# Performance work log

Hardware: AMD Instinct MI355X
Metric: run time of the kernel (lower is better)

The kernel has to match this reference:

```python
import jax, jax.numpy as jnp
import numpy as np


def setup_inputs() -> dict:
    key = jax.random.key(0)
    B, C, T, F = 16, 2, 1000, 257
    k1, = jax.random.split(key, 1)
    inp = jax.random.normal(k1, (B, C, T, F, 2), dtype=jnp.float32)
    weights = jnp.ones((1, C, 1, F, 1), dtype=jnp.float32)   # init constant 1
    bias = jnp.zeros((1, C, 1, F, 1), dtype=jnp.float32)     # init constant 0
    alpha = jnp.full((1, C, F, 1), -4.0, dtype=jnp.float32)  # init constant -4
    s_1 = jnp.zeros((B, C, F, 1), dtype=jnp.float32)
    return {"input": inp, "weights": weights, "bias": bias, "alpha": alpha, "s_1": s_1}


def reference(input, weights, bias, alpha, s_1):
    # input: [B, C, T, F, 2]
    in_data2 = jnp.sum(input ** 2, axis=-1, keepdims=True)  # [B, C, T, F, 1]
    a = jax.nn.sigmoid(alpha)                               # [1, C, F, 1]

    def step(s, x):
        s = s * (1.0 - a) + x * a   # EMA over time, per (c, f)
        return s, s

    # scan over time axis -> move T to leading axis
    xs = jnp.moveaxis(in_data2, 2, 0)          # [T, B, C, F, 1]
    s_last, smooth = jax.lax.scan(step, s_1, xs)
    smooth = jnp.sqrt(jnp.moveaxis(smooth, 0, 2))  # [B, C, T, F, 1]

    res = input / (smooth + 1e-8) * weights + bias
    return res, s_last
```

## Files before the change

### kernel.cpp

```cpp
#include <hip/hip_runtime.h>

#define BB 16
#define CC 2
#define TT 1000
#define FF 257
#define NCHAIN (BB * CC * FF)
#define RES_ELEMS ((size_t)BB * CC * TT * FF * 2)

#define CPB 16
#define KCH 20
#define LCH 50

__global__ __launch_bounds__(320, 3) void fnorm_kernel(
    const float* __restrict__ input,
    const float* __restrict__ weights,
    const float* __restrict__ bias,
    const float* __restrict__ alpha,
    const float* __restrict__ s1,
    float* __restrict__ out)
{
    const int tx = threadIdx.x;
    const int k  = threadIdx.y;
    const int chain = blockIdx.x * CPB + tx;

    const int f  = chain % FF;
    const int bc = chain / FF;
    const int c  = bc % CC;
    const int cf = c * FF + f;

    const float2* __restrict__ in2 = (const float2*)input + (size_t)bc * (TT * FF) + f;
    float2* __restrict__ out2      = (float2*)out        + (size_t)bc * (TT * FF) + f;

    const float av = 1.0f / (1.0f + __expf(-alpha[cf]));
    const float om = 1.0f - av;
    const float w  = weights[cf];
    const float bi = bias[cf];

    const int t0 = k * LCH;

    float2 x[LCH];
    #pragma unroll
    for (int t = 0; t < LCH; ++t) x[t] = in2[(size_t)(t0 + t) * FF];

    float s = 0.0f;
    float p = 1.0f;
    #pragma unroll
    for (int t = 0; t < LCH; ++t) {
        float2 v = x[t];
        float d2 = fmaf(v.x, v.x, v.y * v.y);
        s = fmaf(d2, av, s * om);
        p *= om;
    }

    __shared__ float e_s[KCH][CPB];
    __shared__ float sinit_s[KCH][CPB];
    e_s[k][tx] = s;
    __syncthreads();
    if (k == 0) {
        float S = s1[chain];
        #pragma unroll
        for (int kk = 0; kk < KCH; ++kk) {
            sinit_s[kk][tx] = S;
            S = fmaf(S, p, e_s[kk][tx]);
        }
        out[RES_ELEMS + (size_t)chain] = S;
    }
    __syncthreads();

    s = sinit_s[k][tx];
    #pragma unroll
    for (int t = 0; t < LCH; ++t) {
        float2 v = x[t];
        float d2 = fmaf(v.x, v.x, v.y * v.y);
        s = fmaf(d2, av, s * om);
        float inv = __frsqrt_rn(s + 1e-16f) * w;
        float2 y;
        y.x = fmaf(v.x, inv, bi);
        y.y = fmaf(v.y, inv, bi);
        out2[(size_t)(t0 + t) * FF] = y;
    }
}

extern "C" void kernel_launch(void* const* d_in, const int* in_sizes, int n_in,
                              void* d_out, int out_size, void* d_ws, size_t ws_size,
                              hipStream_t stream) {
    const float* input   = (const float*)d_in[0];
    const float* weights = (const float*)d_in[1];
    const float* bias    = (const float*)d_in[2];
    const float* alpha   = (const float*)d_in[3];
    const float* s1      = (const float*)d_in[4];
    float* out = (float*)d_out;

    dim3 block(CPB, KCH);
    dim3 grid(NCHAIN / CPB);
    hipLaunchKernelGGL(fnorm_kernel, grid, block, 0, stream,
                       input, weights, bias, alpha, s1, out);
}
```

Before: 136.7 us.

## Split time into 64 short chunks and combine chunk carries with wave-wide shuffle scan

Each block now handles 8 chains with 64 time chunks of 16 steps, with bounds guards because 64*16 exceeds 1000. The serial carry combine done by one row of threads is replaced by a Kogge-Stone prefix scan of the (p, e) affine pairs using 64-lane shuffles, one wave per chain. This cuts registers per thread and shortens the serial latency so more waves can be resident. In exchange the scan does extra work, some threads sit idle on the tail chunk, and each row of 8 threads now reads only 8 contiguous float2 per time step, so memory coalescing is narrower.

```diff
diff --git a/kernel.cpp b/kernel.cpp
--- a/kernel.cpp
+++ b/kernel.cpp
@@ -7,11 +7,11 @@
 #define NCHAIN (BB * CC * FF)
 #define RES_ELEMS ((size_t)BB * CC * TT * FF * 2)
 
-#define CPB 16
-#define KCH 20
-#define LCH 50
+#define CPB 8
+#define KCH 64
+#define LCH 16
 
-__global__ __launch_bounds__(320, 3) void fnorm_kernel(
+__global__ __launch_bounds__(512, 8) void fnorm_kernel(
     const float* __restrict__ input,
     const float* __restrict__ weights,
     const float* __restrict__ bias,
@@ -36,48 +36,67 @@
     const float w  = weights[cf];
     const float bi = bias[cf];
 
-    const int t0 = k * LCH;
+    const int t0  = k * LCH;
+    const int rem = TT - t0;
+    const int n   = rem < LCH ? (rem < 0 ? 0 : rem) : LCH;
 
     float2 x[LCH];
     #pragma unroll
-    for (int t = 0; t < LCH; ++t) x[t] = in2[(size_t)(t0 + t) * FF];
+    for (int t = 0; t < LCH; ++t)
+        if (t < n) x[t] = in2[(size_t)(t0 + t) * FF];
 
     float s = 0.0f;
     float p = 1.0f;
     #pragma unroll
     for (int t = 0; t < LCH; ++t) {
-        float2 v = x[t];
-        float d2 = fmaf(v.x, v.x, v.y * v.y);
-        s = fmaf(d2, av, s * om);
-        p *= om;
+        if (t < n) {
+            float2 v = x[t];
+            float d2 = fmaf(v.x, v.x, v.y * v.y);
+            s = fmaf(d2, av, s * om);
+            p *= om;
+        }
     }
 
-    __shared__ float e_s[KCH][CPB];
-    __shared__ float sinit_s[KCH][CPB];
+    __shared__ float p_s[KCH][CPB + 1];
+    __shared__ float e_s[KCH][CPB + 1];
+    __shared__ float i_s[KCH][CPB + 1];
+    p_s[k][tx] = p;
     e_s[k][tx] = s;
     __syncthreads();
-    if (k == 0) {
-        float S = s1[chain];
+    {
+        const int tid = k * CPB + tx;
+        const int wv  = tid >> 6;
+        const int ln  = tid & 63;
+        float pp = p_s[ln][wv];
+        float ee = e_s[ln][wv];
         #pragma unroll
-        for (int kk = 0; kk < KCH; ++kk) {
-            sinit_s[kk][tx] = S;
-            S = fmaf(S, p, e_s[kk][tx]);
+        for (int d = 1; d < 64; d <<= 1) {
+            float pu = __shfl_up(pp, d, 64);
+            float eu = __shfl_up(ee, d, 64);
+            if (ln >= d) { ee = fmaf(pp, eu, ee); pp *= pu; }
         }
-        out[RES_ELEMS + (size_t)chain] = S;
+        const float S0 = s1[blockIdx.x * CPB + wv];
+        float Sin = fmaf(pp, S0, ee);
+        float Sex = __shfl_up(Sin, 1, 64);
+        if (ln == 0) Sex = S0;
+        i_s[ln][wv] = Sex;
+        if (ln == 63) out[RES_ELEMS + (size_t)(blockIdx.x * CPB + wv)] = Sin;
     }
     __syncthreads();
 
-    s = sinit_s[k][tx];
+    s = i_s[k][tx];
     #pragma unroll
     for (int t = 0; t < LCH; ++t) {
-        float2 v = x[t];
-        float d2 = fmaf(v.x, v.x, v.y * v.y);
-        s = fmaf(d2, av, s * om);
-        float inv = __frsqrt_rn(s + 1e-16f) * w;
-        float2 y;
-        y.x = fmaf(v.x, inv, bi);
-        y.y = fmaf(v.y, inv, bi);
-        out2[(size_t)(t0 + t) * FF] = y;
+        if (t < n) {
+            float2 v = x[t];
+            float d2 = fmaf(v.x, v.x, v.y * v.y);
+            s = fmaf(d2, av, s * om);
+            float inv = __frsqrt_rn(s + 1e-16f) * w;
+            float2 y;
+            y.x = fmaf(v.x, inv, bi);
+            y.y = fmaf(v.y, inv, bi);
+            out2[(size_t)(t0 + t) * FF] = y;
+        }
     }
 }
 
```

Measured after the change: 155.5 us. +13.8%, slower.

## Split EMA scan into two kernels with a global chunk-sum workspace

Applied to the files above, without the earlier changes.

Replaces the single fused kernel, which kept 50 time steps per thread in registers and combined chunk carries through shared memory, with two launches. The first computes per-chunk partial EMA sums and writes them to a workspace; the second rebuilds each chunk's starting state from those partials, re-reads the input and writes the normalized output. Work is remapped so each wave covers 64 consecutive frequency bins, giving fully coalesced float2 accesses, with a separate straggler path for the last bin. The aim is better coalescing and occupancy by dropping the large register array, at the cost of reading the input twice and adding an extra launch.

```diff
diff --git a/kernel.cpp b/kernel.cpp
--- a/kernel.cpp
+++ b/kernel.cpp
@@ -4,81 +4,107 @@
 #define CC 2
 #define TT 1000
 #define FF 257
-#define NCHAIN (BB * CC * FF)
+#define NBC (BB * CC)
+#define NCHAIN (NBC * FF)
 #define RES_ELEMS ((size_t)BB * CC * TT * FF * 2)
 
-#define CPB 16
-#define KCH 20
-#define LCH 50
+#define LCH 40
+#define KCH 25
+#define FBLK 4
+#define FULLW (NBC * KCH * FBLK)
+#define STRAG (NBC * KCH)
+#define NTHR 512
+#define WPB (NTHR / 64)
+#define NWAVE (FULLW + (STRAG + 63) / 64)
+#define NBLK ((NWAVE + WPB - 1) / WPB)
 
-__global__ __launch_bounds__(320, 3) void fnorm_kernel(
+__device__ __forceinline__ bool wave_map(int W, int lane,
+                                         int& bc, int& k, int& f) {
+    if (W < FULLW) {
+        bc = W / (KCH * FBLK);
+        const int r = W % (KCH * FBLK);
+        k = r / FBLK;
+        f = (r % FBLK) * 64 + lane;
+        return true;
+    }
+    const int idx = (W - FULLW) * 64 + lane;
+    if (idx < STRAG) { bc = idx / KCH; k = idx % KCH; f = FF - 1; return true; }
+    return false;
+}
+
+__global__ __launch_bounds__(NTHR, 4) void fnorm_sums(
+    const float* __restrict__ input,
+    const float* __restrict__ alpha,
+    float* __restrict__ e_ws)
+{
+    const int W    = blockIdx.x * WPB + (threadIdx.x >> 6);
+    const int lane = threadIdx.x & 63;
+    int bc, k, f;
+    if (!wave_map(W, lane, bc, k, f)) return;
+
+    const int cf = (bc & 1) * FF + f;
+    const float av = 1.0f / (1.0f + __expf(-alpha[cf]));
+    const float om = 1.0f - av;
+
+    const float2* __restrict__ in2 =
+        (const float2*)input + (size_t)bc * (TT * FF) + (size_t)(k * LCH) * FF + f;
+
+    float s = 0.0f;
+    #pragma unroll
+    for (int t = 0; t < LCH; ++t) {
+        float2 v = in2[(size_t)t * FF];
+        s = fmaf(fmaf(v.x, v.x, v.y * v.y), av, s * om);
+    }
+    e_ws[k * NCHAIN + bc * FF + f] = s;
+}
+
+__global__ __launch_bounds__(NTHR, 4) void fnorm_rescan(
     const float* __restrict__ input,
     const float* __restrict__ weights,
     const float* __restrict__ bias,
     const float* __restrict__ alpha,
     const float* __restrict__ s1,
-    float* __restrict__ out)
+    float* __restrict__ out,
+    const float* __restrict__ e_ws)
 {
-    const int tx = threadIdx.x;
-    const int k  = threadIdx.y;
-    const int chain = blockIdx.x * CPB + tx;
+    const int W    = blockIdx.x * WPB + (threadIdx.x >> 6);
+    const int lane = threadIdx.x & 63;
+    int bc, k, f;
+    if (!wave_map(W, lane, bc, k, f)) return;
 
-    const int f  = chain % FF;
-    const int bc = chain / FF;
-    const int c  = bc % CC;
-    const int cf = c * FF + f;
-
-    const float2* __restrict__ in2 = (const float2*)input + (size_t)bc * (TT * FF) + f;
-    float2* __restrict__ out2      = (float2*)out        + (size_t)bc * (TT * FF) + f;
-
+    const int cf = (bc & 1) * FF + f;
     const float av = 1.0f / (1.0f + __expf(-alpha[cf]));
     const float om = 1.0f - av;
     const float w  = weights[cf];
     const float bi = bias[cf];
 
-    const int t0 = k * LCH;
+    const float om2 = om * om, om4 = om2 * om2, om8 = om4 * om4;
+    const float om16 = om8 * om8, om32 = om16 * om16;
+    const float p = om32 * om8;
 
-    float2 x[LCH];
-    #pragma unroll
-    for (int t = 0; t < LCH; ++t) x[t] = in2[(size_t)(t0 + t) * FF];
+    const int chain = bc * FF + f;
+    float S = s1[chain];
+    for (int kk = 0; kk < k; ++kk)
+        S = fmaf(S, p, e_ws[kk * NCHAIN + chain]);
 
-    float s = 0.0f;
-    float p = 1.0f;
+    const size_t base = (size_t)bc * (TT * FF) + (size_t)(k * LCH) * FF + f;
+    const float2* __restrict__ in2  = (const float2*)input + base;
+    float2* __restrict__ out2       = (float2*)out + base;
+
+    float s = S;
     #pragma unroll
     for (int t = 0; t < LCH; ++t) {
-        float2 v = x[t];
-        float d2 = fmaf(v.x, v.x, v.y * v.y);
-        s = fmaf(d2, av, s * om);
-        p *= om;
-    }
-
-    __shared__ float e_s[KCH][CPB];
-    __shared__ float sinit_s[KCH][CPB];
-    e_s[k][tx] = s;
-    __syncthreads();
-    if (k == 0) {
-        float S = s1[chain];
-        #pragma unroll
-        for (int kk = 0; kk < KCH; ++kk) {
-            sinit_s[kk][tx] = S;
-            S = fmaf(S, p, e_s[kk][tx]);
-        }
-        out[RES_ELEMS + (size_t)chain] = S;
-    }
-    __syncthreads();
-
-    s = sinit_s[k][tx];
-    #pragma unroll
-    for (int t = 0; t < LCH; ++t) {
-        float2 v = x[t];
+        float2 v = in2[(size_t)t * FF];
         float d2 = fmaf(v.x, v.x, v.y * v.y);
         s = fmaf(d2, av, s * om);
         float inv = __frsqrt_rn(s + 1e-16f) * w;
         float2 y;
         y.x = fmaf(v.x, inv, bi);
         y.y = fmaf(v.y, inv, bi);
-        out2[(size_t)(t0 + t) * FF] = y;
+        out2[(size_t)t * FF] = y;
     }
+    if (k == KCH - 1)
+        out[RES_ELEMS + (size_t)chain] = s;
 }
 
 extern "C" void kernel_launch(void* const* d_in, const int* in_sizes, int n_in,
@@ -89,10 +115,11 @@
     const float* bias    = (const float*)d_in[2];
     const float* alpha   = (const float*)d_in[3];
     const float* s1      = (const float*)d_in[4];
-    float* out = (float*)d_out;
+    float* out  = (float*)d_out;
+    float* e_ws = (float*)d_ws;
 
-    dim3 block(CPB, KCH);
-    dim3 grid(NCHAIN / CPB);
-    hipLaunchKernelGGL(fnorm_kernel, grid, block, 0, stream,
-                       input, weights, bias, alpha, s1, out);
+    dim3 grid(NBLK), block(NTHR);
+    hipLaunchKernelGGL(fnorm_sums,   grid, block, 0, stream, input, alpha, e_ws);
+    hipLaunchKernelGGL(fnorm_rescan, grid, block, 0, stream,
+                       input, weights, bias, alpha, s1, out, e_ws);
 }
```

Result: slower. 189.8 us (+38.8%).
